# Optimization experiments

Hardware: AMD Instinct MI355X
Metric: run time of the kernel (lower is better)

## Reference

```python
import jax, jax.numpy as jnp
import numpy as np

ML, KS, L = 3, 7, 7  # mL, kernelSize, L = 2*mL+1


def _conv(img, kern, pad, groups=1):
    # img: [N,C,H,W], kern: [O, C//groups, kh, kw]
    return jax.lax.conv_general_dilated(
        img, kern, (1, 1), [(pad, pad), (pad, pad)],
        dimension_numbers=("NCHW", "OIHW", "NCHW"),
        feature_group_count=groups)


def setup_inputs() -> dict:
    key = jax.random.key(0)
    ks = jax.random.split(key, 16)
    B, MU = 64, 256
    lin = lambda k, fi, fo: (jax.random.normal(k, (fi, fo), jnp.float32) / np.sqrt(fi)).astype(jnp.float32)
    return {
        "x": jax.random.normal(ks[0], (B, 1, MU, MU), jnp.float32),
        "f": jax.random.normal(ks[1], (B, 1, MU, MU), jnp.float32),
        "kernelA": jax.random.normal(ks[2], (B, 1, 3, 3), jnp.float32),
        "fc1_w1": lin(ks[3], 9, 200), "fc1_b1": jnp.zeros((200,), jnp.float32),
        "fc1_w2": lin(ks[4], 200, ML * KS * KS), "fc1_b2": jnp.zeros((ML * KS * KS,), jnp.float32),
        "fc2_w1": lin(ks[5], 9, 200), "fc2_b1": jnp.zeros((200,), jnp.float32),
        "fc2_w2": lin(ks[6], 200, ML * ML * KS * KS), "fc2_b2": jnp.zeros((ML * ML * KS * KS,), jnp.float32),
    }


def reference(x, f, kernelA, fc1_w1, fc1_b1, fc1_w2, fc1_b2, fc2_w1, fc2_b1, fc2_w2, fc2_b2):
    B, _, mu, _ = x.shape
    pad = KS // 2

    # residual r = f - A x   (per-sample 3x3 stencil conv, grouped)
    r = f - jax.vmap(lambda xi, ki: _conv(xi[None], ki[None], 1)[0])(x, kernelA)  # [B,1,mu,mu]

    # meta-MLPs produce per-sample dynamic conv kernels from the 3x3 stencil
    kA = kernelA.reshape(B, 9)
    h1 = jax.nn.relu(kA @ fc1_w1 + fc1_b1)
    w1 = (h1 @ fc1_w2 + fc1_b2).reshape(B, ML, 1, KS, KS)
    h2 = jax.nn.relu(kA @ fc2_w1 + fc2_b1)
    w2 = (h2 @ fc2_w2 + fc2_b2).reshape(B, ML, ML, KS, KS)

    # per-sample dynamic convs (batched via vmap)
    G1 = jax.vmap(lambda ri, wi: _conv(ri[None], wi, pad)[0])(r, w1)    # [B,mL,mu,mu]
    G2 = jax.vmap(lambda gi, wi: _conv(gi[None], wi, pad)[0])(G1, w2)   # [B,mL,mu,mu]
    G = jnp.concatenate([r, G1, G2], axis=1)                            # [B,L,mu,mu]

    # S = A G : apply per-sample stencil to each of the L channels (depthwise)
    S = jax.vmap(lambda gi, ki: _conv(gi[None], jnp.broadcast_to(ki[None], (L, 1, 3, 3)), 1, groups=L)[0])(G, kernelA)
    S = S.reshape(B, L, mu * mu)
    Gf = G.reshape(B, L, mu * mu)
    lr = r.reshape(B, mu * mu, 1)

    # normal equations: (S S^T) K = S r, tiny [L,L] solve per sample
    M = jnp.einsum("bln,bmn->blm", S, S)    # [B,L,L]
    b = jnp.matmul(S, lr)                   # [B,L,1]
    K = jnp.linalg.solve(M, b)              # [B,L,1]

    x_new = x + jnp.matmul(K.transpose(0, 2, 1), Gf).reshape(B, 1, mu, mu)
    return x_new
```

## Files before the change

### kernel.cpp

```cpp
#include <hip/hip_runtime.h>
#include <hip/hip_fp16.h>

#define MU 256
#define NPIX (MU*MU)
#define ML 3
#define KS 7
#define LCH 7
#define NENT 35
#define RBLK 64

__device__ __forceinline__ float4 load_h4(const __half* p) {
    __half2 a = *(const __half2*)p;
    __half2 b = *(const __half2*)(p + 2);
    float2 fa = __half22float2(a), fb = __half22float2(b);
    return make_float4(fa.x, fa.y, fb.x, fb.y);
}

__global__ void mlp_kernel(const float* __restrict__ kernelA,
                           const float* __restrict__ fc1_w1, const float* __restrict__ fc1_b1,
                           const float* __restrict__ fc1_w2, const float* __restrict__ fc1_b2,
                           const float* __restrict__ fc2_w1, const float* __restrict__ fc2_b1,
                           const float* __restrict__ fc2_w2, const float* __restrict__ fc2_b2,
                           float* __restrict__ w1_out, float* __restrict__ w2_out) {
    int b = blockIdx.x;
    int t = threadIdx.x;
    __shared__ float kA[9];
    __shared__ float h1[200], h2[200];
    if (t < 9) kA[t] = kernelA[b*9 + t];
    __syncthreads();
    if (t < 200) {
        float s1 = fc1_b1[t], s2 = fc2_b1[t];
        #pragma unroll
        for (int i = 0; i < 9; ++i) {
            s1 += kA[i] * fc1_w1[i*200 + t];
            s2 += kA[i] * fc2_w1[i*200 + t];
        }
        h1[t] = fmaxf(s1, 0.f);
        h2[t] = fmaxf(s2, 0.f);
    }
    __syncthreads();
    if (t < 147) {
        float s = fc1_b2[t];
        for (int i = 0; i < 200; ++i) s += h1[i] * fc1_w2[i*147 + t];
        w1_out[b*147 + t] = s;
    }
    for (int o = t; o < 441; o += 256) {
        float s = fc2_b2[o];
        for (int i = 0; i < 200; ++i) s += h2[i] * fc2_w2[i*441 + o];
        w2_out[b*441 + o] = s;
    }
}

__global__ __launch_bounds__(256) void res_g1_kernel(
        const float* __restrict__ x, const float* __restrict__ f,
        const float* __restrict__ kA, const float* __restrict__ w1,
        __half* __restrict__ r, __half* __restrict__ G1) {
    int b = blockIdx.z;
    __shared__ float xt[24][144];
    __shared__ float rt[22][136];
    int tx = threadIdx.x;
    int ty = threadIdx.y;
    int tid = ty*64 + tx;
    int x0 = blockIdx.x*128, y0 = blockIdx.y*16;
    const float* xb = x + (size_t)b*NPIX;
    const float* fb = f + (size_t)b*NPIX;
    const float* wgt = w1 + (size_t)b*147;
    float k[9];
    #pragma unroll
    for (int i = 0; i < 9; ++i) k[i] = kA[b*9 + i];

    for (int u = tid; u < 24*36; u += 256) {
        int row = u / 36, q4 = u % 36;
        int yy = y0 + row - 4;
        int xx = x0 - 8 + q4*4;
        float4 vv = make_float4(0.f, 0.f, 0.f, 0.f);
        if (yy >= 0 && yy < MU && xx >= 0 && xx < MU)
            vv = *(const float4*)(xb + yy*MU + xx);
        *(float4*)&xt[row][q4*4] = vv;
    }
    __syncthreads();

    for (int u = tid; u < 22*34; u += 256) {
        int row = u / 34, c4 = u % 34;
        int Y = y0 - 3 + row;
        int X = x0 - 4 + 4*c4;
        bool inb = (Y >= 0 && Y < MU && X >= 0 && X < MU);
        float4 fv = make_float4(0.f, 0.f, 0.f, 0.f);
        if (inb) fv = *(const float4*)(fb + Y*MU + X);
        float fr[4] = {fv.x, fv.y, fv.z, fv.w};
        float rr[4];
        #pragma unroll
        for (int cc = 0; cc < 4; ++cc) {
            float s = 0.f;
            #pragma unroll
            for (int di = 0; di < 3; ++di)
                #pragma unroll
                for (int dj = 0; dj < 3; ++dj)
                    s += xt[row + di][4*c4 + 3 + cc + dj] * k[di*3 + dj];
            rr[cc] = inb ? (fr[cc] - s) : 0.f;
        }
        *(float4*)&rt[row][4*c4] = make_float4(rr[0], rr[1], rr[2], rr[3]);
    }
    __syncthreads();

    float accA[3][4], accB[3][4];
    #pragma unroll
    for (int co = 0; co < 3; ++co)
        #pragma unroll
        for (int dy = 0; dy < 4; ++dy) { accA[co][dy] = 0.f; accB[co][dy] = 0.f; }

    int ry = ty*4;
    #pragma unroll
    for (int ir = 0; ir < 10; ++ir) {
        float v[10];
        #pragma unroll
        for (int h = 0; h < 5; ++h)
            *(float2*)&v[h*2] = *(float2*)&rt[ry + ir][2*tx + h*2];
        #pragma unroll
        for (int dy = 0; dy < 4; ++dy) {
            int i = ir - dy;
            if (i >= 0 && i <= 6) {
                #pragma unroll
                for (int co = 0; co < 3; ++co)
                    #pragma unroll
                    for (int j = 0; j < 7; ++j) {
                        float w = wgt[(co*7 + i)*7 + j];
                        accA[co][dy] += v[1 + j] * w;
                        accB[co][dy] += v[2 + j] * w;
                    }
            }
        }
    }
    #pragma unroll
    for (int dy = 0; dy < 4; ++dy) {
        size_t pr = (size_t)b*NPIX + (size_t)(y0 + ry + dy)*MU + x0 + 2*tx;
        float2 rv2 = *(float2*)&rt[3 + ry + dy][4 + 2*tx];
        *(__half2*)&r[pr] = __float22half2_rn(rv2);
        size_t p = (size_t)b*3*NPIX + (size_t)(y0 + ry + dy)*MU + x0 + 2*tx;
        #pragma unroll
        for (int co = 0; co < 3; ++co)
            *(__half2*)&G1[p + (size_t)co*NPIX] =
                __float22half2_rn(make_float2(accA[co][dy], accB[co][dy]));
    }
}

__global__ __launch_bounds__(256) void conv7_g2(
        const __half* __restrict__ G1, const float* __restrict__ w2,
        __half* __restrict__ G2) {
    int b = blockIdx.z;
    __shared__ float tile[3][14][136];
    int tx = threadIdx.x;
    int ty = threadIdx.y;
    int tid = ty*64 + tx;
    int x0 = blockIdx.x*128, y0 = blockIdx.y*8;
    const __half* g1b = G1 + (size_t)b*3*NPIX;
    const float* wgt = w2 + (size_t)b*441;

    for (int u = tid; u < 3*14*34; u += 256) {
        int c = u / (14*34);
        int rem = u % (14*34);
        int row = rem / 34, q4 = rem % 34;
        int yy = y0 + row - 3;
        int xx = x0 - 4 + q4*4;
        float4 vv = make_float4(0.f, 0.f, 0.f, 0.f);
        if (yy >= 0 && yy < MU && xx >= 0 && xx < MU)
            vv = load_h4(g1b + (size_t)c*NPIX + yy*MU + xx);
        *(float4*)&tile[c][row][q4*4] = vv;
    }
    __syncthreads();

    float accA[3][2], accB[3][2];
    #pragma unroll
    for (int co = 0; co < 3; ++co)
        #pragma unroll
        for (int dy = 0; dy < 2; ++dy) { accA[co][dy] = 0.f; accB[co][dy] = 0.f; }

    int ry = ty*2;
    #pragma unroll
    for (int c = 0; c < 3; ++c) {
        #pragma unroll
        for (int ir = 0; ir < 8; ++ir) {
            float v[10];
            #pragma unroll
            for (int h = 0; h < 5; ++h)
                *(float2*)&v[h*2] = *(float2*)&tile[c][ry + ir][2*tx + h*2];
            #pragma unroll
            for (int dy = 0; dy < 2; ++dy) {
                int i = ir - dy;
                if (i >= 0 && i <= 6) {
                    #pragma unroll
                    for (int co = 0; co < 3; ++co)
                        #pragma unroll
                        for (int j = 0; j < 7; ++j) {
                            float w = wgt[((co*3 + c)*7 + i)*7 + j];
                            accA[co][dy] += v[1 + j] * w;
                            accB[co][dy] += v[2 + j] * w;
                        }
                }
            }
        }
    }
    #pragma unroll
    for (int dy = 0; dy < 2; ++dy) {
        size_t p = (size_t)b*3*NPIX + (size_t)(y0 + ry + dy)*MU + x0 + 2*tx;
        #pragma unroll
        for (int co = 0; co < 3; ++co)
            *(__half2*)&G2[p + (size_t)co*NPIX] =
                __float22half2_rn(make_float2(accA[co][dy], accB[co][dy]));
    }
}

__global__ __launch_bounds__(256, 4) void reduce_kernel(
        const __half* __restrict__ r, const __half* __restrict__ G1,
        const __half* __restrict__ G2, const float* __restrict__ kA,
        float* __restrict__ partial) {
    int b = blockIdx.z;
    __shared__ float tile[7][18][72];
    __shared__ float wsum[NENT][4];
    int tx = threadIdx.x;
    int ty = threadIdx.y;
    int tid = ty*64 + tx;
    float k[9];
    #pragma unroll
    for (int i = 0; i < 9; ++i) k[i] = kA[b*9 + i];

    const __half* srcs[7] = {
        r  + (size_t)b*NPIX,
        G1 + (size_t)b*3*NPIX, G1 + (size_t)b*3*NPIX + NPIX, G1 + (size_t)b*3*NPIX + 2*NPIX,
        G2 + (size_t)b*3*NPIX, G2 + (size_t)b*3*NPIX + NPIX, G2 + (size_t)b*3*NPIX + 2*NPIX
    };

    int x0 = blockIdx.x*64;
    int ysub = blockIdx.y*16;

    #pragma unroll
    for (int c = 0; c < 7; ++c) {
        const __half* src = srcs[c];
        for (int u = tid; u < 18*18; u += 256) {
            int row = u / 18, q4 = u % 18;
            int yy = ysub + row - 1;
            int xx = x0 - 4 + q4*4;
            float4 vv = make_float4(0.f, 0.f, 0.f, 0.f);
            if (yy >= 0 && yy < MU && xx >= 0 && xx < MU)
                vv = load_h4(src + yy*MU + xx);
            *(float4*)&tile[c][row][q4*4] = vv;
        }
    }
    __syncthreads();

    float acc[64];
    #pragma unroll
    for (int e = 0; e < 64; ++e) acc[e] = 0.f;

    int ry = ty*4;
    float S_all[7][4];
    #pragma unroll
    for (int c = 0; c < 7; ++c) {
        float S0 = 0.f, S1 = 0.f, S2 = 0.f, S3 = 0.f;
        #pragma unroll
        for (int t = 0; t < 6; ++t) {
            float v0 = tile[c][ry + t][tx + 3];
            float v1 = tile[c][ry + t][tx + 4];
            float v2 = tile[c][ry + t][tx + 5];
            float e0 = v0*k[0] + v1*k[1] + v2*k[2];
            float e1 = v0*k[3] + v1*k[4] + v2*k[5];
            float e2 = v0*k[6] + v1*k[7] + v2*k[8];
            if (t == 0) { S0 += e0; }
            if (t == 1) { S1 += e0; S0 += e1; }
            if (t == 2) { S2 += e0; S1 += e1; S0 += e2; }
            if (t == 3) { S3 += e0; S2 += e1; S1 += e2; }
            if (t == 4) {           S3 += e1; S2 += e2; }
            if (t == 5) {                     S3 += e2; }
        }
        S_all[c][0] = S0; S_all[c][1] = S1; S_all[c][2] = S2; S_all[c][3] = S3;
    }
    #pragma unroll
    for (int dy = 0; dy < 4; ++dy) {
        float rv = tile[0][ry + dy + 1][tx + 4];
        int idx = 0;
        #pragma unroll
        for (int l = 0; l < 7; ++l) {
            #pragma unroll
            for (int m = l; m < 7; ++m) {
                acc[idx] += S_all[l][dy] * S_all[m][dy];
                ++idx;
            }
        }
        #pragma unroll
        for (int l = 0; l < 7; ++l) acc[28 + l] += S_all[l][dy] * rv;
    }

    #pragma unroll
    for (int step = 0; step < 6; ++step) {
        const int mask = 1 << step;
        const int nh = 32 >> step;
        bool hi = (tx & mask) != 0;
        #pragma unroll
        for (int i = 0; i < nh; ++i) {
            float send = hi ? acc[i] : acc[i + nh];
            float got = __shfl_xor(send, mask);
            acc[i] = (hi ? acc[i + nh] : acc[i]) + got;
        }
    }
    int ent = ((tx&1)<<5) | ((tx&2)<<3) | ((tx&4)<<1)
            | ((tx&8)>>1) | ((tx&16)>>3) | ((tx&32)>>5);
    if (ent < NENT) wsum[ent][ty] = acc[0];
    __syncthreads();
    if (tid < NENT) {
        float s = wsum[tid][0] + wsum[tid][1] + wsum[tid][2] + wsum[tid][3];
        int blockLinear = blockIdx.y*4 + blockIdx.x;
        partial[((size_t)b*NENT + tid)*RBLK + blockLinear] = s;
    }
}

__global__ void reduce2_kernel(const float* __restrict__ partial,
                               double* __restrict__ M, double* __restrict__ bv) {
    int b = blockIdx.x;
    int wave = threadIdx.x >> 6;
    int lane = threadIdx.x & 63;
    for (int e = wave; e < NENT; e += 4) {
        const float* p = partial + ((size_t)b*NENT + e)*RBLK;
        double s = (double)p[lane];
        #pragma unroll
        for (int off = 32; off; off >>= 1) s += __shfl_down(s, off);
        if (lane == 0) {
            if (e < 28) M[b*28 + e] = s;
            else        bv[b*7 + (e - 28)] = s;
        }
    }
}

__global__ __launch_bounds__(64, 1) void solve_kernel(
        const double* __restrict__ M, const double* __restrict__ bv,
        float* __restrict__ K, int B) {
    int b = blockIdx.x*64 + threadIdx.x;
    if (b >= B) return;
    double A[7][8];
    int idx = 0;
    #pragma unroll
    for (int l = 0; l < 7; ++l)
        #pragma unroll
        for (int m = l; m < 7; ++m) {
            double v = M[b*28 + idx];
            A[l][m] = v;
            A[m][l] = v;
            ++idx;
        }
    #pragma unroll
    for (int l = 0; l < 7; ++l) A[l][7] = bv[b*7 + l];

    #pragma unroll
    for (int col = 0; col < 7; ++col) {
        int piv = col;
        double mx = fabs(A[col][col]);
        #pragma unroll
        for (int rr = 0; rr < 7; ++rr) {
            if (rr > col) {
                double a = fabs(A[rr][col]);
                if (a > mx) { mx = a; piv = rr; }
            }
        }
        #pragma unroll
        for (int rr = 0; rr < 7; ++rr) {
            if (rr > col) {
                bool c = (rr == piv);
                #pragma unroll
                for (int cc = 0; cc < 8; ++cc) {
                    double t0 = A[col][cc], t1 = A[rr][cc];
                    A[col][cc] = c ? t1 : t0;
                    A[rr][cc]  = c ? t0 : t1;
                }
            }
        }
        double d = A[col][col];
        #pragma unroll
        for (int rr = 0; rr < 7; ++rr) {
            if (rr > col) {
                double fct = A[rr][col] / d;
                #pragma unroll
                for (int cc = 0; cc < 8; ++cc) A[rr][cc] -= fct * A[col][cc];
            }
        }
    }
    double Kv[7];
    #pragma unroll
    for (int rr = 6; rr >= 0; --rr) {
        double s = A[rr][7];
        #pragma unroll
        for (int cc = 0; cc < 7; ++cc)
            if (cc > rr) s -= A[rr][cc] * Kv[cc];
        Kv[rr] = s / A[rr][rr];
    }
    #pragma unroll
    for (int l = 0; l < 7; ++l) K[b*7 + l] = (float)Kv[l];
}

__global__ void update_kernel(const float* __restrict__ x, const __half* __restrict__ r,
                              const __half* __restrict__ G1, const __half* __restrict__ G2,
                              const float* __restrict__ K, float* __restrict__ out) {
    int b = blockIdx.z;
    int p4 = blockIdx.x*256 + threadIdx.x;
    float k0 = K[b*7+0], k1 = K[b*7+1], k2 = K[b*7+2], k3 = K[b*7+3];
    float k4 = K[b*7+4], k5 = K[b*7+5], k6 = K[b*7+6];
    size_t q  = (size_t)b*(NPIX/4) + p4;
    size_t e0 = ((size_t)b*3*NPIX) + (size_t)p4*4;
    size_t er = ((size_t)b*NPIX) + (size_t)p4*4;

    float4 xv = ((const float4*)x)[q];
    float4 rv; { float4 t = load_h4(r + er); rv = t; }
    float4 a  = load_h4(G1 + e0);
    float4 bb = load_h4(G1 + e0 + NPIX);
    float4 c  = load_h4(G1 + e0 + 2*(size_t)NPIX);
    float4 d  = load_h4(G2 + e0);
    float4 e  = load_h4(G2 + e0 + NPIX);
    float4 g  = load_h4(G2 + e0 + 2*(size_t)NPIX);
    float4 o;
    o.x = xv.x + k0*rv.x + k1*a.x + k2*bb.x + k3*c.x + k4*d.x + k5*e.x + k6*g.x;
    o.y = xv.y + k0*rv.y + k1*a.y + k2*bb.y + k3*c.y + k4*d.y + k5*e.y + k6*g.y;
    o.z = xv.z + k0*rv.z + k1*a.z + k2*bb.z + k3*c.z + k4*d.z + k5*e.z + k6*g.z;
    o.w = xv.w + k0*rv.w + k1*a.w + k2*bb.w + k3*c.w + k4*d.w + k5*e.w + k6*g.w;
    ((float4*)out)[q] = o;
}

extern "C" void kernel_launch(void* const* d_in, const int* in_sizes, int n_in,
                              void* d_out, int out_size, void* d_ws, size_t ws_size,
                              hipStream_t stream) {
    const float* x       = (const float*)d_in[0];
    const float* f       = (const float*)d_in[1];
    const float* kernelA = (const float*)d_in[2];
    const float* fc1_w1  = (const float*)d_in[3];
    const float* fc1_b1  = (const float*)d_in[4];
    const float* fc1_w2  = (const float*)d_in[5];
    const float* fc1_b2  = (const float*)d_in[6];
    const float* fc2_w1  = (const float*)d_in[7];
    const float* fc2_b1  = (const float*)d_in[8];
    const float* fc2_w2  = (const float*)d_in[9];
    const float* fc2_b2  = (const float*)d_in[10];
    float* out = (float*)d_out;

    const int B = in_sizes[2] / 9;

    double* Mws = (double*)d_ws;
    double* bws = Mws + (size_t)B*28;
    float*  w1  = (float*)(bws + (size_t)B*7);
    float*  w2  = w1 + (size_t)B*147;
    float*  Kv  = w2 + (size_t)B*441;
    float*  partial = Kv + (size_t)B*7;
    __half* r   = (__half*)(partial + (size_t)B*NENT*RBLK);
    __half* G1  = r  + (size_t)B*NPIX;
    __half* G2  = G1 + (size_t)B*3*NPIX;

    dim3 cblk(64, 4);
    dim3 rgrd(MU/64, MU/16, B);
    dim3 g1grd(MU/128, MU/16, B);
    dim3 g2grd(MU/128, MU/8, B);

    hipLaunchKernelGGL(mlp_kernel, dim3(B), dim3(256), 0, stream,
                       kernelA, fc1_w1, fc1_b1, fc1_w2, fc1_b2,
                       fc2_w1, fc2_b1, fc2_w2, fc2_b2, w1, w2);
    hipLaunchKernelGGL(res_g1_kernel, g1grd, cblk, 0, stream, x, f, kernelA, w1, r, G1);
    hipLaunchKernelGGL(conv7_g2, g2grd, cblk, 0, stream, G1, w2, G2);
    hipLaunchKernelGGL(reduce_kernel, rgrd, cblk, 0, stream, r, G1, G2, kernelA, partial);
    hipLaunchKernelGGL(reduce2_kernel, dim3(B), dim3(256), 0, stream, partial, Mws, bws);
    hipLaunchKernelGGL(solve_kernel, dim3((B + 63)/64), dim3(64), 0, stream, Mws, bws, Kv, B);
    hipLaunchKernelGGL(update_kernel, dim3(NPIX/1024, 1, B), dim3(256), 0, stream,
                       x, r, G1, G2, Kv, out);
}
```

Before: 178.1 us.

## Use packed fp16 dot2 for the G2 7x7 conv with pre-packed weights

The MLP now writes the 3x3x7x7 second-stage weights as pre-shifted fp16 pairs (zero-padded for odd and even output alignment). The G2 convolution keeps its input tile in fp16 shared memory and accumulates with v_dot2 fp16-to-fp32 instructions, roughly halving the multiply-add count and shared-memory footprint. Weights lose precision by being rounded to fp16, and the tile load now skips the half-to-float conversion.

```diff
diff --git a/kernel.cpp b/kernel.cpp
--- a/kernel.cpp
+++ b/kernel.cpp
@@ -9,6 +9,16 @@
 #define NENT 35
 #define RBLK 64
 
+typedef _Float16 half2r __attribute__((ext_vector_type(2)));
+
+__device__ __forceinline__ float dot2f(half2r a, half2r b, float c) {
+#if __has_builtin(__builtin_amdgcn_fdot2)
+    return __builtin_amdgcn_fdot2(a, b, c, false);
+#else
+    return c + (float)a.x*(float)b.x + (float)a.y*(float)b.y;
+#endif
+}
+
 __device__ __forceinline__ float4 load_h4(const __half* p) {
     __half2 a = *(const __half2*)p;
     __half2 b = *(const __half2*)(p + 2);
@@ -21,11 +31,12 @@
                            const float* __restrict__ fc1_w2, const float* __restrict__ fc1_b2,
                            const float* __restrict__ fc2_w1, const float* __restrict__ fc2_b1,
                            const float* __restrict__ fc2_w2, const float* __restrict__ fc2_b2,
-                           float* __restrict__ w1_out, float* __restrict__ w2_out) {
+                           float* __restrict__ w1_out, half2r* __restrict__ w2p) {
     int b = blockIdx.x;
     int t = threadIdx.x;
     __shared__ float kA[9];
     __shared__ float h1[200], h2[200];
+    __shared__ float w2s[441];
     if (t < 9) kA[t] = kernelA[b*9 + t];
     __syncthreads();
     if (t < 200) {
@@ -47,7 +58,18 @@
     for (int o = t; o < 441; o += 256) {
         float s = fc2_b2[o];
         for (int i = 0; i < 200; ++i) s += h2[i] * fc2_w2[i*441 + o];
-        w2_out[b*441 + o] = s;
+        w2s[o] = s;
+    }
+    __syncthreads();
+    for (int u = t; u < 504; u += 256) {
+        int grp = u / 8, p = u % 8;
+        int co = grp % 3, i = (grp / 3) % 7, c = grp / 21;
+        const float* w = &w2s[co*147 + c*49 + i*7];
+        float lo, hi;
+        if (p < 4) { lo = (p == 0) ? 0.f : w[2*p - 1]; hi = w[2*p]; }
+        else       { int q = p - 4; lo = w[2*q]; hi = (q == 3) ? 0.f : w[2*q + 1]; }
+        half2r hp; hp.x = (_Float16)lo; hp.y = (_Float16)hi;
+        w2p[(size_t)b*504 + u] = hp;
     }
 }
 
@@ -145,16 +167,16 @@
 }
 
 __global__ __launch_bounds__(256) void conv7_g2(
-        const __half* __restrict__ G1, const float* __restrict__ w2,
+        const __half* __restrict__ G1, const half2r* __restrict__ w2p,
         __half* __restrict__ G2) {
     int b = blockIdx.z;
-    __shared__ float tile[3][14][136];
+    __shared__ _Float16 tile[3][14][136];
     int tx = threadIdx.x;
     int ty = threadIdx.y;
     int tid = ty*64 + tx;
     int x0 = blockIdx.x*128, y0 = blockIdx.y*8;
     const __half* g1b = G1 + (size_t)b*3*NPIX;
-    const float* wgt = w2 + (size_t)b*441;
+    const half2r* wp = w2p + (size_t)b*504;
 
     for (int u = tid; u < 3*14*34; u += 256) {
         int c = u / (14*34);
@@ -162,10 +184,10 @@
         int row = rem / 34, q4 = rem % 34;
         int yy = y0 + row - 3;
         int xx = x0 - 4 + q4*4;
-        float4 vv = make_float4(0.f, 0.f, 0.f, 0.f);
+        ushort4 vv = make_ushort4(0, 0, 0, 0);
         if (yy >= 0 && yy < MU && xx >= 0 && xx < MU)
-            vv = load_h4(g1b + (size_t)c*NPIX + yy*MU + xx);
-        *(float4*)&tile[c][row][q4*4] = vv;
+            vv = *(const ushort4*)(g1b + (size_t)c*NPIX + yy*MU + xx);
+        *(ushort4*)&tile[c][row][q4*4] = vv;
     }
     __syncthreads();
 
@@ -180,22 +202,26 @@
     for (int c = 0; c < 3; ++c) {
         #pragma unroll
         for (int ir = 0; ir < 8; ++ir) {
-            float v[10];
+            half2r P[5];
             #pragma unroll
-            for (int h = 0; h < 5; ++h)
-                *(float2*)&v[h*2] = *(float2*)&tile[c][ry + ir][2*tx + h*2];
+            for (int q = 0; q < 5; ++q)
+                P[q] = *(const half2r*)&tile[c][ry + ir][2*tx + 2*q];
             #pragma unroll
             for (int dy = 0; dy < 2; ++dy) {
                 int i = ir - dy;
                 if (i >= 0 && i <= 6) {
                     #pragma unroll
-                    for (int co = 0; co < 3; ++co)
-                        #pragma unroll
-                        for (int j = 0; j < 7; ++j) {
-                            float w = wgt[((co*3 + c)*7 + i)*7 + j];
-                            accA[co][dy] += v[1 + j] * w;
-                            accB[co][dy] += v[2 + j] * w;
-                        }
+                    for (int co = 0; co < 3; ++co) {
+                        const half2r* wv = wp + ((c*7 + i)*3 + co)*8;
+                        accA[co][dy] = dot2f(P[0], wv[0], accA[co][dy]);
+                        accA[co][dy] = dot2f(P[1], wv[1], accA[co][dy]);
+                        accA[co][dy] = dot2f(P[2], wv[2], accA[co][dy]);
+                        accA[co][dy] = dot2f(P[3], wv[3], accA[co][dy]);
+                        accB[co][dy] = dot2f(P[1], wv[4], accB[co][dy]);
+                        accB[co][dy] = dot2f(P[2], wv[5], accB[co][dy]);
+                        accB[co][dy] = dot2f(P[3], wv[6], accB[co][dy]);
+                        accB[co][dy] = dot2f(P[4], wv[7], accB[co][dy]);
+                    }
                 }
             }
         }
@@ -407,7 +433,7 @@
     size_t er = ((size_t)b*NPIX) + (size_t)p4*4;
 
     float4 xv = ((const float4*)x)[q];
-    float4 rv; { float4 t = load_h4(r + er); rv = t; }
+    float4 rv = load_h4(r + er);
     float4 a  = load_h4(G1 + e0);
     float4 bb = load_h4(G1 + e0 + NPIX);
     float4 c  = load_h4(G1 + e0 + 2*(size_t)NPIX);
@@ -440,15 +466,15 @@
 
     const int B = in_sizes[2] / 9;
 
-    double* Mws = (double*)d_ws;
-    double* bws = Mws + (size_t)B*28;
-    float*  w1  = (float*)(bws + (size_t)B*7);
-    float*  w2  = w1 + (size_t)B*147;
-    float*  Kv  = w2 + (size_t)B*441;
-    float*  partial = Kv + (size_t)B*7;
-    __half* r   = (__half*)(partial + (size_t)B*NENT*RBLK);
-    __half* G1  = r  + (size_t)B*NPIX;
-    __half* G2  = G1 + (size_t)B*3*NPIX;
+    double*  Mws = (double*)d_ws;
+    double*  bws = Mws + (size_t)B*28;
+    float*   w1  = (float*)(bws + (size_t)B*7);
+    float*   Kv  = w1 + (size_t)B*147;
+    float*   partial = Kv + (size_t)B*7;
+    half2r*  w2p = (half2r*)(partial + (size_t)B*NENT*RBLK);
+    __half*  r   = (__half*)(w2p + (size_t)B*504);
+    __half*  G1  = r  + (size_t)B*NPIX;
+    __half*  G2  = G1 + (size_t)B*3*NPIX;
 
     dim3 cblk(64, 4);
     dim3 rgrd(MU/64, MU/16, B);
@@ -457,9 +483,9 @@
 
     hipLaunchKernelGGL(mlp_kernel, dim3(B), dim3(256), 0, stream,
                        kernelA, fc1_w1, fc1_b1, fc1_w2, fc1_b2,
-                       fc2_w1, fc2_b1, fc2_w2, fc2_b2, w1, w2);
+                       fc2_w1, fc2_b1, fc2_w2, fc2_b2, w1, w2p);
     hipLaunchKernelGGL(res_g1_kernel, g1grd, cblk, 0, stream, x, f, kernelA, w1, r, G1);
-    hipLaunchKernelGGL(conv7_g2, g2grd, cblk, 0, stream, G1, w2, G2);
+    hipLaunchKernelGGL(conv7_g2, g2grd, cblk, 0, stream, G1, w2p, G2);
     hipLaunchKernelGGL(reduce_kernel, rgrd, cblk, 0, stream, r, G1, G2, kernelA, partial);
     hipLaunchKernelGGL(reduce2_kernel, dim3(B), dim3(256), 0, stream, partial, Mws, bws);
     hipLaunchKernelGGL(solve_kernel, dim3((B + 63)/64), dim3(64), 0, stream, Mws, bws, Kv, B);
```

Result: faster. 169.4 us (-4.9%).
